# Optimization experiments

Hardware: AMD Instinct MI355X
Metric: run time of the kernel (lower is better)

## Reference

```python
import jax, jax.numpy as jnp
import numpy as np
import math

ROPE_BASE = 10000.0

def rope(x):
    # rotate-half RoPE over the full feature dim. x: [B, S, D]
    B, S, D = x.shape
    half = D // 2
    inv_freq = 1.0 / (ROPE_BASE ** (jnp.arange(half, dtype=jnp.float32) / half))
    ang = jnp.arange(S, dtype=jnp.float32)[:, None] * inv_freq[None, :]  # [S, half]
    cos, sin = jnp.cos(ang), jnp.sin(ang)
    x1, x2 = x[..., :half], x[..., half:]
    return jnp.concatenate([x1 * cos - x2 * sin, x1 * sin + x2 * cos], axis=-1)

def setup_inputs() -> dict:
    key = jax.random.key(0)
    ks = jax.random.split(key, 10)
    B, S, D = 4, 2048, 2048
    scale = 1.0 / math.sqrt(D)
    x = jax.random.normal(ks[0], (B, S, D), dtype=jnp.float32)
    mask = jnp.broadcast_to(jnp.tril(jnp.ones((S, S), dtype=jnp.int32)), (B, S, S))
    Wq = jax.random.normal(ks[1], (D, D), dtype=jnp.float32) * scale
    bq = jax.random.normal(ks[2], (D,), dtype=jnp.float32) * 0.02
    Wk = jax.random.normal(ks[3], (D, D), dtype=jnp.float32) * scale
    bk = jax.random.normal(ks[4], (D,), dtype=jnp.float32) * 0.02
    Wv = jax.random.normal(ks[5], (D, D), dtype=jnp.float32) * scale
    bv = jax.random.normal(ks[6], (D,), dtype=jnp.float32) * 0.02
    Wo = jax.random.normal(ks[7], (D, D), dtype=jnp.float32) * scale
    bo = jax.random.normal(ks[8], (D,), dtype=jnp.float32) * 0.02
    return {"x": x, "mask": mask, "Wq": Wq, "bq": bq, "Wk": Wk, "bk": bk,
            "Wv": Wv, "bv": bv, "Wo": Wo, "bo": bo}

def reference(x, mask, Wq, bq, Wk, bk, Wv, bv, Wo, bo):
    # x: [B, S, D]; torch.nn.Linear convention: y = x @ W.T + b
    D = x.shape[-1]
    std = jnp.sqrt(jnp.asarray(D, dtype=x.dtype))
    q = jnp.einsum('bsd,ed->bse', x, Wq) + bq
    k = jnp.einsum('bsd,ed->bse', x, Wk) + bk
    v = jnp.einsum('bsd,ed->bse', x, Wv) + bv
    # cache=None prefill path: q sliced to last x.size(-2) positions (full seq here)
    Sq = x.shape[-2]
    q = rope(q)[:, -Sq:, :]
    k = rope(k)
    scores = jnp.einsum('bqd,bkd->bqk', q, k) / std  # [B, Sq, Sk]
    scores = jnp.where(mask[:, -Sq:, :] == 0, -jnp.inf, scores)
    attn = jax.nn.softmax(scores, axis=-1)  # dropout=0 (eval)
    ctx = jnp.einsum('bqk,bkd->bqd', attn, v)
    out = jnp.einsum('bqd,ed->bqe', ctx, Wo) + bo
    return out
```

## Files before the change

kernel.cpp:

```cpp
#include <hip/hip_runtime.h>
#include <stdint.h>
#include <math.h>

#define BLK 256

typedef __bf16 bf16x8 __attribute__((ext_vector_type(8)));
typedef float  f32x4  __attribute__((ext_vector_type(4)));

__device__ __forceinline__ uint16_t f2bf(float f) {
  uint32_t u = __float_as_uint(f);
  u += 0x7fffu + ((u >> 16) & 1u);
  return (uint16_t)(u >> 16);
}
__device__ __forceinline__ float bf2f(uint16_t h) {
  return __uint_as_float(((uint32_t)h) << 16);
}

__device__ __forceinline__ void load_lds16(const void* g, void* l) {
  __builtin_amdgcn_global_load_lds(
      (const __attribute__((address_space(1))) uint32_t*)g,
      (__attribute__((address_space(3))) uint32_t*)l,
      16, 0, 0);
}

#define MFMA16(a, b, c) __builtin_amdgcn_mfma_f32_16x16x32_bf16(a, b, c, 0, 0, 0)

__global__ __launch_bounds__(BLK)
void convert_all(const float* __restrict__ x, const float* __restrict__ wq,
                 const float* __restrict__ wk, const float* __restrict__ wv,
                 const float* __restrict__ wo,
                 uint16_t* __restrict__ xb, uint16_t* __restrict__ wqkv,
                 float* __restrict__ sums) {
  const long tid0 = (long)blockIdx.x * BLK + threadIdx.x;
  if (tid0 < 8192) sums[tid0] = 0.f;
  const long XG = 4194304;
  const long T  = XG + 4 * 1048576;
  for (long i = tid0; i < T; i += (long)gridDim.x * BLK) {
    const float* src; uint16_t* dst; long off, doff;
    if (i < XG) { src = x; dst = xb; off = i; doff = i; }
    else {
      const long j = i - XG;
      const int seg = (int)(j >> 20);
      off = j & 1048575;
      src = (seg == 0) ? wq : (seg == 1) ? wk : (seg == 2) ? wv : wo;
      dst = wqkv + ((long)seg << 22);
      if (seg < 2) {
        const int f = (int)(off >> 9);
        const int g = (int)(off & 511);
        const int c = (f < 1024) ? (f << 1) : (((f - 1024) << 1) | 1);
        doff = (long)c * 512 + g;
      } else doff = off;
    }
    float4 v = ((const float4*)src)[off];
    ushort4 o;
    o.x = f2bf(v.x); o.y = f2bf(v.y); o.z = f2bf(v.z); o.w = f2bf(v.w);
    ((ushort4*)dst)[doff] = o;
  }
}

template<int MODE>
__global__ __launch_bounds__(512, 2)
void gemm256(const uint16_t* __restrict__ A, const uint16_t* __restrict__ Bt,
             const float* __restrict__ b0, const float* __restrict__ b1,
             const float* __restrict__ b2, void* __restrict__ Cv,
             uint16_t* __restrict__ Vt)
{
  constexpr int LD = 2048;
  constexpr int NT = 32;
  extern __shared__ ulonglong2 smem_raw[];
  uint16_t* smem = (uint16_t*)smem_raw;

  const int tid  = threadIdx.x;
  const int lane = tid & 63;
  const int wave = tid >> 6;
  const int quad = lane >> 4;
  const int l16  = lane & 15;
  const int rsw  = (l16 >> 1) & 3;

  const int nx   = gridDim.x;
  const int nwg  = nx * gridDim.y;
  const int wgid = blockIdx.y * nx + blockIdx.x;
  const int sw   = (wgid & 7) * (nwg >> 3) + (wgid >> 3);
  const int tile_n = (sw % nx) << 8;
  const int tile_m = (sw / nx) << 8;

  const int wm = (wave & 1) << 7;
  const int wn = (wave >> 1) << 6;

  const int srow = tid >> 2;
  const int wch  = (((tid & 3) ^ ((tid >> 3) & 3)) << 3);
  const uint16_t* gA = A  + (long)(tile_m + srow) * LD + wch;
  const uint16_t* gB = Bt + (long)(tile_n + srow) * LD + wch;

  f32x4 acc[8][4];
#pragma unroll
  for (int i = 0; i < 8; ++i)
#pragma unroll
    for (int j = 0; j < 4; ++j) acc[i][j] = (f32x4){0.f, 0.f, 0.f, 0.f};

  auto stage2 = [&](int bufoff, const uint16_t* g0, int moff, int s, int kk) {
    const uint16_t* g = g0 + kk + s * 32;
    uint16_t* l = smem + bufoff + moff + s * 8192 + (wave << 9);
    load_lds16(g, l);
    load_lds16(g + 128 * LD, l + 4096);
  };

  const int raoff = (wm + l16) * 32;
  const int rboff = 16384 + (wn + l16) * 32;
  const int psw   = (quad ^ rsw) << 3;

  stage2(0, gA, 0, 0, 0); stage2(0, gB, 16384, 0, 0);
  stage2(0, gA, 0, 1, 0); stage2(0, gB, 16384, 1, 0);
  asm volatile("s_waitcnt vmcnt(0)" ::: "memory");
  __builtin_amdgcn_s_barrier();
  asm volatile("" ::: "memory");

  for (int t = 0; t < NT; ++t) {
    const int cur = (t & 1) << 15;
    const int oth = 32768 - cur;
    const int kk1 = (t + 1) << 6;
    const bool pf = (t + 1 < NT);
    const uint16_t* bc = smem + cur;
    bf16x8 af[8], bq0, bq1;

    if (pf) stage2(oth, gA, 0, 0, kk1);
    if (pf) { asm volatile("s_waitcnt vmcnt(6)" ::: "memory"); }
    else    { asm volatile("s_waitcnt vmcnt(4)" ::: "memory"); }
    __builtin_amdgcn_s_barrier();
    asm volatile("" ::: "memory");
#pragma unroll
    for (int mi = 0; mi < 8; ++mi)
      af[mi] = *(const bf16x8*)(bc + raoff + mi * 512 + psw);
    bq0 = *(const bf16x8*)(bc + rboff + 0 * 512 + psw);
    bq1 = *(const bf16x8*)(bc + rboff + 1 * 512 + psw);
    __builtin_amdgcn_s_setprio(1);
#pragma unroll
    for (int mi = 0; mi < 8; ++mi) {
      acc[mi][0] = MFMA16(af[mi], bq0, acc[mi][0]);
      acc[mi][1] = MFMA16(af[mi], bq1, acc[mi][1]);
    }
    __builtin_amdgcn_s_setprio(0);
    __builtin_amdgcn_s_barrier();

    if (pf) stage2(oth, gB, 16384, 0, kk1);
    bq0 = *(const bf16x8*)(bc + rboff + 2 * 512 + psw);
    bq1 = *(const bf16x8*)(bc + rboff + 3 * 512 + psw);
    __builtin_amdgcn_s_setprio(1);
#pragma unroll
    for (int mi = 0; mi < 8; ++mi) {
      acc[mi][2] = MFMA16(af[mi], bq0, acc[mi][2]);
      acc[mi][3] = MFMA16(af[mi], bq1, acc[mi][3]);
    }
    __builtin_amdgcn_s_setprio(0);
    __builtin_amdgcn_s_barrier();

    if (pf) stage2(oth, gA, 0, 1, kk1);
    if (pf) { asm volatile("s_waitcnt vmcnt(6)" ::: "memory"); }
    else    { asm volatile("s_waitcnt vmcnt(0)" ::: "memory"); }
    __builtin_amdgcn_s_barrier();
    asm volatile("" ::: "memory");
#pragma unroll
    for (int mi = 0; mi < 8; ++mi)
      af[mi] = *(const bf16x8*)(bc + 8192 + raoff + mi * 512 + psw);
    bq0 = *(const bf16x8*)(bc + 8192 + rboff + 0 * 512 + psw);
    bq1 = *(const bf16x8*)(bc + 8192 + rboff + 1 * 512 + psw);
    __builtin_amdgcn_s_setprio(1);
#pragma unroll
    for (int mi = 0; mi < 8; ++mi) {
      acc[mi][0] = MFMA16(af[mi], bq0, acc[mi][0]);
      acc[mi][1] = MFMA16(af[mi], bq1, acc[mi][1]);
    }
    __builtin_amdgcn_s_setprio(0);
    __builtin_amdgcn_s_barrier();

    if (pf) stage2(oth, gB, 16384, 1, kk1);
    bq0 = *(const bf16x8*)(bc + 8192 + rboff + 2 * 512 + psw);
    bq1 = *(const bf16x8*)(bc + 8192 + rboff + 3 * 512 + psw);
    __builtin_amdgcn_s_setprio(1);
#pragma unroll
    for (int mi = 0; mi < 8; ++mi) {
      acc[mi][2] = MFMA16(af[mi], bq0, acc[mi][2]);
      acc[mi][3] = MFMA16(af[mi], bq1, acc[mi][3]);
    }
    __builtin_amdgcn_s_setprio(0);
    __builtin_amdgcn_s_barrier();
  }

  const int crow0 = tile_m + wm + (quad << 2);
  const int ccol0 = tile_n + wn + l16;

  if constexpr (MODE == 1) {
    const int seg = tile_n >> 11;
    if (seg < 2) {
      const float* bp = seg ? b1 : b0;
      uint16_t* Cp = (uint16_t*)Cv;
#pragma unroll
      for (int ni = 0; ni < 4; ++ni) {
        const int col = ccol0 + ni * 16;
        const int cc = col & 2047;
        const float bb = bp[(cc >> 1) + (cc & 1) * 1024];
        const float invf = exp2f((float)(cc >> 1) * (-13.287712379549449f / 1024.f));
        const float sgn = (cc & 1) ? 1.f : -1.f;
#pragma unroll
        for (int mi = 0; mi < 8; ++mi) {
#pragma unroll
          for (int r = 0; r < 4; ++r) {
            const int row = crow0 + mi * 16 + r;
            const float v = acc[mi][ni][r] + bb;
            float sn, cs;
            __sincosf((float)(row & 2047) * invf, &sn, &cs);
            const float p = __shfl_xor(v, 1, 64);
            Cp[(long)row * 4096 + col] = f2bf(v * cs + p * sgn * sn);
          }
        }
      }
    } else {
      uint16_t* ws = smem + wave * 8192;
#pragma unroll
      for (int ni = 0; ni < 4; ++ni) {
        const int f = ni * 16 + l16;
        const float bb = b2[(ccol0 + ni * 16) & 2047];
#pragma unroll
        for (int mi = 0; mi < 8; ++mi) {
          const int t0 = mi * 16 + (quad << 2);
          union { uint16_t u16[4]; uint64_t u64; } pk;
#pragma unroll
          for (int r = 0; r < 4; ++r) pk.u16[r] = f2bf(acc[mi][ni][r] + bb);
          *(uint64_t*)(ws + f * 128 + (t0 ^ ((f & 15) << 3))) = pk.u64;
        }
      }
      __syncthreads();
      const int bno      = (tile_m + wm) >> 11;
      const int tokbase  = (tile_m + wm) & 2047;
      const int featbase = tile_n - 4096 + wn;
      uint16_t* Vp = Vt + (long)bno * 4194304 + tokbase;
#pragma unroll
      for (int jj = 0; jj < 16; ++jj) {
        const int f = jj * 4 + quad;
        const uint16_t* srcp = ws + f * 128 + ((l16 * 8) ^ ((f & 15) << 3));
        ulonglong2 v = *(const ulonglong2*)srcp;
        *(ulonglong2*)(Vp + (long)(featbase + f) * 2048 + l16 * 8) = v;
      }
    }
  } else {
    float* Co = (float*)Cv;
#pragma unroll
    for (int ni = 0; ni < 4; ++ni) {
      const int col = ccol0 + ni * 16;
      const float bb = b0[col];
#pragma unroll
      for (int mi = 0; mi < 8; ++mi)
#pragma unroll
        for (int r = 0; r < 4; ++r)
          Co[(long)(crow0 + mi * 16 + r) * 2048 + col] = acc[mi][ni][r] + bb;
    }
  }
}

template<int MODE, int MINW>
__global__ __launch_bounds__(BLK, MINW)
void gemm_bt(const uint16_t* __restrict__ A, int lda,
             const uint16_t* __restrict__ Bt, int ldb,
             const float* __restrict__ b0, const float* __restrict__ b1,
             const float* __restrict__ b2,
             void* __restrict__ Cv, int ldc,
             int K, long sAb, long sBb, long sCb,
             float scale, float* __restrict__ rowsum,
             uint16_t* __restrict__ Vt)
{
  int tile_m, tile_n, bz;
  if (MODE == 2) {
    const int t = blockIdx.x;
    int r = (int)((sqrtf(8.f * (float)t + 1.f) - 1.f) * 0.5f);
    while ((r + 1) * (r + 2) / 2 <= t) ++r;
    while (r * (r + 1) / 2 > t) --r;
    tile_m = r * 128;
    tile_n = (t - r * (r + 1) / 2) * 128;
    bz = blockIdx.z;
  } else if (MODE == 3) {
    bz = blockIdx.y & 3;
    tile_m = ((int)(gridDim.y >> 2) - 1 - (int)(blockIdx.y >> 2)) * 128;
    tile_n = blockIdx.x * 128;
  } else {
    tile_m = blockIdx.y * 128;
    tile_n = blockIdx.x * 128;
    bz = blockIdx.z;
  }
  A  += (long)bz * sAb;
  Bt += (long)bz * sBb;

  __shared__ __align__(16) uint16_t smem[16384];
  uint16_t* sA = smem;
  uint16_t* sB = smem + 8192;

  const int tid  = threadIdx.x;
  const int lane = tid & 63;
  const int wave = tid >> 6;
  const int quad = lane >> 4;
  const int l16  = lane & 15;
  const int x8   = l16 & 7;
  const int wm = (wave & 1) * 64;
  const int wn = (wave >> 1) * 64;

  f32x4 acc[4][4];
#pragma unroll
  for (int i = 0; i < 4; ++i)
#pragma unroll
    for (int j = 0; j < 4; ++j) acc[i][j] = (f32x4){0.f, 0.f, 0.f, 0.f};

  const uint16_t* gA[4]; const uint16_t* gB[4];
  uint16_t* lA[4]; uint16_t* lB[4];
#pragma unroll
  for (int i = 0; i < 4; ++i) {
    const int id = wave * 256 + i * 64 + lane;
    const int row = id >> 3;
    const int c = (id & 7) ^ (row & 7);
    gA[i] = A  + (long)(tile_m + row) * lda + c * 8;
    gB[i] = Bt + (long)(tile_n + row) * ldb + c * 8;
    lA[i] = sA + (wave * 256 + i * 64) * 8;
    lB[i] = sB + (wave * 256 + i * 64) * 8;
  }

  const int kend = (MODE == 3) ? min(K, tile_m + 128) : K;

  for (int kk = 0; kk < kend; kk += 64) {
#pragma unroll
    for (int i = 0; i < 4; ++i) {
      load_lds16(gA[i] + kk, lA[i]);
      load_lds16(gB[i] + kk, lB[i]);
    }
    __syncthreads();

#pragma unroll
    for (int s2 = 0; s2 < 2; ++s2) {
      const int slot = ((quad + s2 * 4) ^ x8) * 8;
      bf16x8 af[4], bfr[4];
#pragma unroll
      for (int mi = 0; mi < 4; ++mi)
        af[mi] = *(const bf16x8*)(sA + (wm + mi * 16 + l16) * 64 + slot);
#pragma unroll
      for (int ni = 0; ni < 4; ++ni)
        bfr[ni] = *(const bf16x8*)(sB + (wn + ni * 16 + l16) * 64 + slot);
#pragma unroll
      for (int mi = 0; mi < 4; ++mi)
#pragma unroll
        for (int ni = 0; ni < 4; ++ni)
          acc[mi][ni] = MFMA16(af[mi], bfr[ni], acc[mi][ni]);
    }
    __syncthreads();
  }

  const int crow0 = tile_m + wm + quad * 4;
  const int ccol0 = tile_n + wn + l16;

  if constexpr (MODE == 2) {
    const bool diag = (tile_m == tile_n);
    uint16_t* Pp = (uint16_t*)Cv + (long)bz * sCb;
    float* rs = rowsum + (long)bz * 2048;
#pragma unroll
    for (int mi = 0; mi < 4; ++mi) {
#pragma unroll
      for (int r = 0; r < 4; ++r) {
        const int row = crow0 + mi * 16 + r;
        float partial = 0.f;
#pragma unroll
        for (int ni = 0; ni < 4; ++ni) {
          const int col = ccol0 + ni * 16;
          const float e = (!diag || col <= row) ? __expf(acc[mi][ni][r] * scale) : 0.f;
          const uint16_t h = f2bf(e);
          partial += bf2f(h);
          Pp[(long)row * ldc + col] = h;
        }
#pragma unroll
        for (int o = 1; o < 16; o <<= 1) partial += __shfl_xor(partial, o, 64);
        if (l16 == 0) atomicAdd(rs + row, partial);
      }
    }
  } else if constexpr (MODE == 3) {
    uint16_t* Cp = (uint16_t*)Cv + (long)bz * sCb;
    const float* rs = rowsum + (long)bz * 2048;
#pragma unroll
    for (int mi = 0; mi < 4; ++mi) {
#pragma unroll
      for (int r = 0; r < 4; ++r) {
        const int row = crow0 + mi * 16 + r;
        const float inv = 1.f / rs[row];
#pragma unroll
        for (int ni = 0; ni < 4; ++ni)
          Cp[(long)row * ldc + ccol0 + ni * 16] = f2bf(acc[mi][ni][r] * inv);
      }
    }
  }
}

extern "C" void kernel_launch(void* const* d_in, const int* in_sizes, int n_in,
                              void* d_out, int out_size, void* d_ws, size_t ws_size,
                              hipStream_t stream) {
  const long S = 2048, D = 2048;
  const long MD = 4 * S * D;
  const long DD = D * D;

  const float* x  = (const float*)d_in[0];
  const float* Wq = (const float*)d_in[2];
  const float* bq = (const float*)d_in[3];
  const float* Wk = (const float*)d_in[4];
  const float* bk = (const float*)d_in[5];
  const float* Wv = (const float*)d_in[6];
  const float* bv = (const float*)d_in[7];
  const float* Wo = (const float*)d_in[8];
  const float* bo = (const float*)d_in[9];

  uint16_t* Xb    = (uint16_t*)d_ws;
  uint16_t* Wqkvb = Xb + MD;
  uint16_t* QK    = Wqkvb + 4 * DD;
  uint16_t* Vt    = QK + 8192L * 4096;
  uint16_t* P     = Vt + MD;
  float*    sums  = (float*)(P + 4 * S * S);
  if (ws_size < 268435456ull) return;

  static int once = []() {
    hipFuncSetAttribute(reinterpret_cast<const void*>(&gemm256<1>),
                        hipFuncAttributeMaxDynamicSharedMemorySize, 131072);
    hipFuncSetAttribute(reinterpret_cast<const void*>(&gemm256<0>),
                        hipFuncAttributeMaxDynamicSharedMemorySize, 131072);
    return 0;
  }();
  (void)once;

  dim3 blk(BLK);

  convert_all<<<16384, blk, 0, stream>>>(x, Wq, Wk, Wv, Wo, Xb, Wqkvb, sums);

  gemm256<1><<<dim3(24, 32), dim3(512), 131072, stream>>>(
      Xb, Wqkvb, bq, bk, bv, QK, Vt);

  gemm_bt<2, 3><<<dim3(136, 1, 4), blk, 0, stream>>>(
      QK, 4096, QK + 2048, 4096, nullptr, nullptr, nullptr, P, 2048,
      2048, 2048L * 4096, 2048L * 4096, S * S,
      0.022097086912079608f, sums, nullptr);

  gemm_bt<3, 4><<<dim3(16, 64, 1), blk, 0, stream>>>(
      P, 2048, Vt, 2048, nullptr, nullptr, nullptr, Xb, 2048,
      2048, S * S, S * D, S * D, 1.f, sums, nullptr);

  gemm256<0><<<dim3(8, 32), dim3(512), 131072, stream>>>(
      Xb, Wqkvb + 3 * DD, bo, nullptr, nullptr, (float*)d_out, nullptr);
}
```

Measured before the change: 610.3 us.

## Deepen GEMM prefetch to two K-tiles ahead and regroup XCD tile mapping

```diff
diff --git a/kernel.cpp b/kernel.cpp
--- a/kernel.cpp
+++ b/kernel.cpp
@@ -77,12 +77,15 @@
   const int l16  = lane & 15;
   const int rsw  = (l16 >> 1) & 3;
 
-  const int nx   = gridDim.x;
-  const int nwg  = nx * gridDim.y;
+  const int nx = gridDim.x;
+  const int ny = gridDim.y;
   const int wgid = blockIdx.y * nx + blockIdx.x;
-  const int sw   = (wgid & 7) * (nwg >> 3) + (wgid >> 3);
-  const int tile_n = (sw % nx) << 8;
-  const int tile_m = (sw / nx) << 8;
+  const int xcd  = wgid & 7;
+  const int r    = wgid >> 3;
+  const int PM = ny >> 2;
+  const int PN = nx >> 1;
+  const int tile_m = (((xcd >> 1) * PM + r / PN) << 8);
+  const int tile_n = (((xcd & 1) * PN + r % PN) << 8);
 
   const int wm = (wave & 1) << 7;
   const int wn = (wave >> 1) << 6;
@@ -98,91 +101,114 @@
 #pragma unroll
     for (int j = 0; j < 4; ++j) acc[i][j] = (f32x4){0.f, 0.f, 0.f, 0.f};
 
-  auto stage2 = [&](int bufoff, const uint16_t* g0, int moff, int s, int kk) {
-    const uint16_t* g = g0 + kk + s * 32;
-    uint16_t* l = smem + bufoff + moff + s * 8192 + (wave << 9);
-    load_lds16(g, l);
-    load_lds16(g + 128 * LD, l + 4096);
+  auto stage8 = [&](int bufoff, int kk) {
+#pragma unroll
+    for (int s = 0; s < 2; ++s) {
+      const uint16_t* g = gA + kk + s * 32;
+      uint16_t* l = smem + bufoff + s * 8192 + (wave << 9);
+      load_lds16(g, l);
+      load_lds16(g + 128 * LD, l + 4096);
+    }
+#pragma unroll
+    for (int s = 0; s < 2; ++s) {
+      const uint16_t* g = gB + kk + s * 32;
+      uint16_t* l = smem + bufoff + 16384 + s * 8192 + (wave << 9);
+      load_lds16(g, l);
+      load_lds16(g + 128 * LD, l + 4096);
+    }
   };
 
-  const int raoff = (wm + l16) * 32;
-  const int rboff = 16384 + (wn + l16) * 32;
-  const int psw   = (quad ^ rsw) << 3;
-
-  stage2(0, gA, 0, 0, 0); stage2(0, gB, 16384, 0, 0);
-  stage2(0, gA, 0, 1, 0); stage2(0, gB, 16384, 1, 0);
-  asm volatile("s_waitcnt vmcnt(0)" ::: "memory");
+  const int psw = (quad ^ rsw) << 3;
+
+  stage8(0, 0);
+  stage8(32768, 64);
+  asm volatile("s_waitcnt vmcnt(8)" ::: "memory");
   __builtin_amdgcn_s_barrier();
-  asm volatile("" ::: "memory");
+
+  bf16x8 aR[4][2], bR[4][2];
 
   for (int t = 0; t < NT; ++t) {
     const int cur = (t & 1) << 15;
-    const int oth = 32768 - cur;
-    const int kk1 = (t + 1) << 6;
-    const bool pf = (t + 1 < NT);
     const uint16_t* bc = smem + cur;
-    bf16x8 af[8], bq0, bq1;
-
-    if (pf) stage2(oth, gA, 0, 0, kk1);
-    if (pf) { asm volatile("s_waitcnt vmcnt(6)" ::: "memory"); }
-    else    { asm volatile("s_waitcnt vmcnt(4)" ::: "memory"); }
-    __builtin_amdgcn_s_barrier();
-    asm volatile("" ::: "memory");
-#pragma unroll
-    for (int mi = 0; mi < 8; ++mi)
-      af[mi] = *(const bf16x8*)(bc + raoff + mi * 512 + psw);
-    bq0 = *(const bf16x8*)(bc + rboff + 0 * 512 + psw);
-    bq1 = *(const bf16x8*)(bc + rboff + 1 * 512 + psw);
+    const uint16_t* pA = bc + (wm + l16) * 32 + psw;
+    const uint16_t* pB = bc + 16384 + (wn + l16) * 32 + psw;
+
+#pragma unroll
+    for (int mi = 0; mi < 4; ++mi) {
+      aR[mi][0] = *(const bf16x8*)(pA + mi * 512);
+      aR[mi][1] = *(const bf16x8*)(pA + mi * 512 + 8192);
+    }
+#pragma unroll
+    for (int ni = 0; ni < 2; ++ni) {
+      bR[ni][0] = *(const bf16x8*)(pB + ni * 512);
+      bR[ni][1] = *(const bf16x8*)(pB + ni * 512 + 8192);
+    }
+    __builtin_amdgcn_s_barrier();
+    asm volatile("s_waitcnt lgkmcnt(0)" ::: "memory");
+    __builtin_amdgcn_sched_barrier(0);
     __builtin_amdgcn_s_setprio(1);
 #pragma unroll
-    for (int mi = 0; mi < 8; ++mi) {
-      acc[mi][0] = MFMA16(af[mi], bq0, acc[mi][0]);
-      acc[mi][1] = MFMA16(af[mi], bq1, acc[mi][1]);
-    }
+    for (int ks = 0; ks < 2; ++ks)
+#pragma unroll
+      for (int mi = 0; mi < 4; ++mi)
+#pragma unroll
+        for (int ni = 0; ni < 2; ++ni)
+          acc[mi][ni] = MFMA16(aR[mi][ks], bR[ni][ks], acc[mi][ni]);
     __builtin_amdgcn_s_setprio(0);
     __builtin_amdgcn_s_barrier();
 
-    if (pf) stage2(oth, gB, 16384, 0, kk1);
-    bq0 = *(const bf16x8*)(bc + rboff + 2 * 512 + psw);
-    bq1 = *(const bf16x8*)(bc + rboff + 3 * 512 + psw);
+#pragma unroll
+    for (int ni = 2; ni < 4; ++ni) {
+      bR[ni][0] = *(const bf16x8*)(pB + ni * 512);
+      bR[ni][1] = *(const bf16x8*)(pB + ni * 512 + 8192);
+    }
+    __builtin_amdgcn_s_barrier();
+    asm volatile("s_waitcnt lgkmcnt(0)" ::: "memory");
+    __builtin_amdgcn_sched_barrier(0);
     __builtin_amdgcn_s_setprio(1);
 #pragma unroll
-    for (int mi = 0; mi < 8; ++mi) {
-      acc[mi][2] = MFMA16(af[mi], bq0, acc[mi][2]);
-      acc[mi][3] = MFMA16(af[mi], bq1, acc[mi][3]);
-    }
+    for (int ks = 0; ks < 2; ++ks)
+#pragma unroll
+      for (int mi = 0; mi < 4; ++mi)
+#pragma unroll
+        for (int ni = 2; ni < 4; ++ni)
+          acc[mi][ni] = MFMA16(aR[mi][ks], bR[ni][ks], acc[mi][ni]);
     __builtin_amdgcn_s_setprio(0);
     __builtin_amdgcn_s_barrier();
 
-    if (pf) stage2(oth, gA, 0, 1, kk1);
-    if (pf) { asm volatile("s_waitcnt vmcnt(6)" ::: "memory"); }
-    else    { asm volatile("s_waitcnt vmcnt(0)" ::: "memory"); }
-    __builtin_amdgcn_s_barrier();
-    asm volatile("" ::: "memory");
-#pragma unroll
-    for (int mi = 0; mi < 8; ++mi)
-      af[mi] = *(const bf16x8*)(bc + 8192 + raoff + mi * 512 + psw);
-    bq0 = *(const bf16x8*)(bc + 8192 + rboff + 0 * 512 + psw);
-    bq1 = *(const bf16x8*)(bc + 8192 + rboff + 1 * 512 + psw);
+#pragma unroll
+    for (int mi = 0; mi < 4; ++mi) {
+      aR[mi][0] = *(const bf16x8*)(pA + 2048 + mi * 512);
+      aR[mi][1] = *(const bf16x8*)(pA + 2048 + mi * 512 + 8192);
+    }
+    __builtin_amdgcn_s_barrier();
+    asm volatile("s_waitcnt lgkmcnt(0)" ::: "memory");
+    __builtin_amdgcn_sched_barrier(0);
     __builtin_amdgcn_s_setprio(1);
 #pragma unroll
-    for (int mi = 0; mi < 8; ++mi) {
-      acc[mi][0] = MFMA16(af[mi], bq0, acc[mi][0]);
-      acc[mi][1] = MFMA16(af[mi], bq1, acc[mi][1]);
-    }
+    for (int ks = 0; ks < 2; ++ks)
+#pragma unroll
+      for (int mi = 0; mi < 4; ++mi)
+#pragma unroll
+        for (int ni = 0; ni < 2; ++ni)
+          acc[mi + 4][ni] = MFMA16(aR[mi][ks], bR[ni][ks], acc[mi + 4][ni]);
     __builtin_amdgcn_s_setprio(0);
     __builtin_amdgcn_s_barrier();
 
-    if (pf) stage2(oth, gB, 16384, 1, kk1);
-    bq0 = *(const bf16x8*)(bc + 8192 + rboff + 2 * 512 + psw);
-    bq1 = *(const bf16x8*)(bc + 8192 + rboff + 3 * 512 + psw);
+    if (t + 2 < NT) stage8(cur, (t + 2) << 6);
+    __builtin_amdgcn_sched_barrier(0);
     __builtin_amdgcn_s_setprio(1);
 #pragma unroll
-    for (int mi = 0; mi < 8; ++mi) {
-      acc[mi][2] = MFMA16(af[mi], bq0, acc[mi][2]);
-      acc[mi][3] = MFMA16(af[mi], bq1, acc[mi][3]);
-    }
+    for (int ks = 0; ks < 2; ++ks)
+#pragma unroll
+      for (int mi = 0; mi < 4; ++mi)
+#pragma unroll
+        for (int ni = 2; ni < 4; ++ni)
+          acc[mi + 4][ni] = MFMA16(aR[mi][ks], bR[ni][ks], acc[mi + 4][ni]);
     __builtin_amdgcn_s_setprio(0);
+    __builtin_amdgcn_sched_barrier(0);
+    if (t + 2 < NT) { asm volatile("s_waitcnt vmcnt(8)" ::: "memory"); }
+    else            { asm volatile("s_waitcnt vmcnt(0)" ::: "memory"); }
     __builtin_amdgcn_s_barrier();
   }
 
```

New measurement: 631.5 us. 3.5% more time.
